# Performance work log

Hardware: AMD Instinct MI355X
Metric: run time of the kernel (lower is better)

The kernel has to match this reference:

```python
import jax, jax.numpy as jnp
import numpy as np

H = 2048        # hidden_size
NH = 16         # query heads
NKV = 4         # kv heads (= NH//4, from k_proj shape H x H//4)
HD = H // NH    # head_dim = 128
B, S = 2, 2048
SCALE = 1.0 / (HD ** 0.5)


def _rope(x, cos, sin):
    # x: [B, h, S, d]; cos/sin: [S, d//2]; rotate complex pairs (even, odd)
    xr = x[..., 0::2]
    xi = x[..., 1::2]
    c = cos[None, None, :x.shape[2], :]
    s = sin[None, None, :x.shape[2], :]
    out_r = xr * c - xi * s
    out_i = xr * s + xi * c
    return jnp.stack([out_r, out_i], axis=-1).reshape(x.shape)


def setup_inputs() -> dict:
    key = jax.random.key(0)
    ks = jax.random.split(key, 6)
    hidden_states = jax.random.normal(ks[0], (B, S, H), dtype=jnp.float32)
    # RoPE table (theta = 10000), head_dim//2 frequencies
    inv_freq = 1.0 / (10000.0 ** (np.arange(0, HD, 2, dtype=np.float32) / HD))
    angles = np.arange(S, dtype=np.float32)[:, None] * inv_freq[None, :]
    freqs_cos = jnp.asarray(np.cos(angles), dtype=jnp.float32)
    freqs_sin = jnp.asarray(np.sin(angles), dtype=jnp.float32)
    w = 0.02  # keep activations in a sane range
    Wq = jax.random.normal(ks[1], (H, H), dtype=jnp.float32) * w
    Wk = jax.random.normal(ks[2], (H // 4, H), dtype=jnp.float32) * w
    Wv = jax.random.normal(ks[3], (H // 4, H), dtype=jnp.float32) * w
    Wo = jax.random.normal(ks[4], (H, H), dtype=jnp.float32) * w
    return {"hidden_states": hidden_states, "freqs_cos": freqs_cos,
            "freqs_sin": freqs_sin, "Wq": Wq, "Wk": Wk, "Wv": Wv, "Wo": Wo}


def reference(hidden_states, freqs_cos, freqs_sin, Wq, Wk, Wv, Wo):
    b, s, _ = hidden_states.shape
    q = hidden_states @ Wq.T                      # [B,S,H]
    k = hidden_states @ Wk.T                      # [B,S,H/4]
    v = hidden_states @ Wv.T                      # [B,S,H/4]
    q = q.reshape(b, s, NH, HD).transpose(0, 2, 1, 3)    # [B,NH,S,HD]
    k = k.reshape(b, s, NKV, HD).transpose(0, 2, 1, 3)   # [B,NKV,S,HD]
    v = v.reshape(b, s, NKV, HD).transpose(0, 2, 1, 3)
    q = _rope(q, freqs_cos, freqs_sin)
    k = _rope(k, freqs_cos, freqs_sin)
    # GQA: each kv head serves NH//NKV query heads
    k_rep = jnp.repeat(k, NH // NKV, axis=1)      # [B,NH,S,HD]
    v_rep = jnp.repeat(v, NH // NKV, axis=1)
    scores = jnp.einsum('bhqd,bhkd->bhqk', q, k_rep) * SCALE  # [B,NH,S,S]
    probs = jax.nn.softmax(scores, axis=-1)
    out = jnp.einsum('bhqk,bhkd->bhqd', probs, v_rep)         # [B,NH,S,HD]
    out = out.transpose(0, 2, 1, 3).reshape(b, s, H)
    return out @ Wo.T
```

## Files before the change

kernel.cpp:

```cpp
#include <hip/hip_runtime.h>

typedef __bf16 bf16_t;
typedef bf16_t bf16x8 __attribute__((ext_vector_type(8)));
typedef bf16_t bf16x2 __attribute__((ext_vector_type(2)));
typedef float f32x4 __attribute__((ext_vector_type(4)));
typedef unsigned int u32x4 __attribute__((ext_vector_type(4)));

typedef const __attribute__((address_space(1))) void* as1_cvp;
typedef __attribute__((address_space(3))) void* as3_vp;

__device__ __forceinline__ void gload16(const void* g, void* l) {
  __builtin_amdgcn_global_load_lds((as1_cvp)g, (as3_vp)l, 16, 0, 0);
}

__global__ __launch_bounds__(256) void cvt_kernel(const float* __restrict__ src,
                                                  bf16_t* __restrict__ dst, int n8) {
  int i = blockIdx.x * 256 + threadIdx.x;
  if (i >= n8) return;
  int idx = i * 8;
  float4 a = *(const float4*)(src + idx);
  float4 b = *(const float4*)(src + idx + 4);
  bf16x8 o;
  o[0] = (bf16_t)a.x; o[1] = (bf16_t)a.y; o[2] = (bf16_t)a.z; o[3] = (bf16_t)a.w;
  o[4] = (bf16_t)b.x; o[5] = (bf16_t)b.y; o[6] = (bf16_t)b.z; o[7] = (bf16_t)b.w;
  *(bf16x8*)(dst + idx) = o;
}

#define BM 128
#define BN 128
#define BK 64
__global__ __launch_bounds__(256, 2) void gemm_bt(const bf16_t* __restrict__ A,
                                                  const bf16_t* __restrict__ B,
                                                  float* __restrict__ C,
                                                  int M, int N, int K) {
  __shared__ alignas(16) bf16_t As[BM * BK];
  __shared__ alignas(16) bf16_t Bs[BN * BK];
  const int t = threadIdx.x;
  const int lane = t & 63, w = t >> 6;
  const int wm = w >> 1, wn = w & 1;
  const int lr = lane & 15, lg = lane >> 4;
  const int m0 = blockIdx.y * BM, n0 = blockIdx.x * BN;
  const int srow = t >> 3, scol = (t & 7) * 8;

  f32x4 acc[4][4] = {};

  for (int kb = 0; kb < K; kb += BK) {
    __syncthreads();
#pragma unroll
    for (int i = 0; i < 4; ++i) {
      gload16(A + (size_t)(m0 + srow + 32 * i) * K + kb + scol, As + i * 2048 + t * 8);
      gload16(B + (size_t)(n0 + srow + 32 * i) * K + kb + scol, Bs + i * 2048 + t * 8);
    }
    __syncthreads();
#pragma unroll
    for (int kk = 0; kk < 2; ++kk) {
      const int ko = kk * 32 + lg * 8;
      bf16x8 af[4], bfr[4];
#pragma unroll
      for (int r = 0; r < 4; ++r)
        af[r] = *(const bf16x8*)(As + (wm * 64 + r * 16 + lr) * BK + ko);
#pragma unroll
      for (int c = 0; c < 4; ++c)
        bfr[c] = *(const bf16x8*)(Bs + (wn * 64 + c * 16 + lr) * BK + ko);
#pragma unroll
      for (int r = 0; r < 4; ++r)
#pragma unroll
        for (int c = 0; c < 4; ++c)
          acc[r][c] = __builtin_amdgcn_mfma_f32_16x16x32_bf16(af[r], bfr[c], acc[r][c], 0, 0, 0);
    }
  }
#pragma unroll
  for (int r = 0; r < 4; ++r)
#pragma unroll
    for (int c = 0; c < 4; ++c)
#pragma unroll
      for (int b = 0; b < 4; ++b)
        C[(size_t)(m0 + wm * 64 + r * 16 + lg * 4 + b) * N + n0 + wn * 64 + c * 16 + lr] =
            acc[r][c][b];
}

__global__ __launch_bounds__(256) void rope_kernel(const float* __restrict__ qkv,
                                                   const float* __restrict__ cs,
                                                   const float* __restrict__ sn,
                                                   bf16_t* __restrict__ dst,
                                                   int nh, int lognh, int col_off) {
  int idx = blockIdx.x * 256 + threadIdx.x;
  int chunk = idx & 15;
  int s = (idx >> 4) & 2047;
  int hh = (idx >> 15) & (nh - 1);
  int bb = idx >> (15 + lognh);
  const float* src = qkv + (size_t)(bb * 2048 + s) * 3072 + col_off + hh * 128 + chunk * 8;
  float4 x0 = *(const float4*)src;
  float4 x1 = *(const float4*)(src + 4);
  float4 c4 = *(const float4*)(cs + s * 64 + chunk * 4);
  float4 s4 = *(const float4*)(sn + s * 64 + chunk * 4);
  bf16x8 o;
  o[0] = (bf16_t)(x0.x * c4.x - x0.y * s4.x);
  o[1] = (bf16_t)(x0.x * s4.x + x0.y * c4.x);
  o[2] = (bf16_t)(x0.z * c4.y - x0.w * s4.y);
  o[3] = (bf16_t)(x0.z * s4.y + x0.w * c4.y);
  o[4] = (bf16_t)(x1.x * c4.z - x1.y * s4.z);
  o[5] = (bf16_t)(x1.x * s4.z + x1.y * c4.z);
  o[6] = (bf16_t)(x1.z * c4.w - x1.w * s4.w);
  o[7] = (bf16_t)(x1.z * s4.w + x1.w * c4.w);
  *(bf16x8*)(dst + ((size_t)(bb * nh + hh) * 2048 + s) * 128 + chunk * 8) = o;
}

__global__ __launch_bounds__(256) void vt_kernel(const float* __restrict__ qkv,
                                                 bf16_t* __restrict__ vt) {
  __shared__ bf16_t tile[64][128];
  int t = threadIdx.x;
  int bid = blockIdx.x;
  int st = bid & 31;
  int kh = (bid >> 5) & 3;
  int bb = bid >> 7;
  const float* src = qkv + (size_t)(bb * 2048 + st * 64) * 3072 + 2560 + kh * 128;
#pragma unroll
  for (int j = 0; j < 8; ++j) {
    int id = t + 256 * j;
    int sr = id >> 5, dv = id & 31;
    float4 x = *(const float4*)(src + (size_t)sr * 3072 + dv * 4);
    tile[sr][dv * 4 + 0] = (bf16_t)x.x;
    tile[sr][dv * 4 + 1] = (bf16_t)x.y;
    tile[sr][dv * 4 + 2] = (bf16_t)x.z;
    tile[sr][dv * 4 + 3] = (bf16_t)x.w;
  }
  __syncthreads();
  bf16_t* dst = vt + (size_t)(bb * 4 + kh) * 128 * 2048 + st * 64;
#pragma unroll
  for (int j = 0; j < 4; ++j) {
    int id = t + 256 * j;
    int d = id >> 3, sc8 = id & 7;
    bf16x8 v;
#pragma unroll
    for (int e = 0; e < 8; ++e) v[e] = tile[sc8 * 8 + e][d];
    *(bf16x8*)(dst + (size_t)d * 2048 + sc8 * 8) = v;
  }
}

#define KVB 64
__global__ __launch_bounds__(256, 3) void attn_kernel(const bf16_t* __restrict__ Q,
                                                      const bf16_t* __restrict__ Kg,
                                                      const bf16_t* __restrict__ Vg,
                                                      bf16_t* __restrict__ O) {
  __shared__ alignas(16) bf16_t Ks[2][KVB * 128];
  __shared__ alignas(16) bf16_t Vs[128 * KVB];
  const int t = threadIdx.x;
  const int lane = t & 63, w = t >> 6;
  const int lr = lane & 15, lg = lane >> 4;
  const int swz = (lr & 7) * 8;
  const int bid = blockIdx.x;
  const int qt = bid & 31;
  const int h = (bid >> 5) & 15;
  const int bb = bid >> 9;
  const int kvh = h >> 2;

  const bf16_t* Qh = Q + (((size_t)bb * 16 + h) * 2048 + qt * 64 + w * 16) * 128;
  const bf16_t* Kh = Kg + ((size_t)bb * 4 + kvh) * 2048 * 128;
  const bf16_t* Vh = Vg + ((size_t)bb * 4 + kvh) * 128 * 2048;

  const int krow = t >> 4;
  const int kcs = ((t & 15) ^ (krow & 7)) * 8;
  const int vrow = t >> 3;
  const int vcs = ((t & 7) ^ (vrow & 7)) * 8;

  bf16x8 qf[4];
#pragma unroll
  for (int kc = 0; kc < 4; ++kc)
    qf[kc] = *(const bf16x8*)(Qh + lr * 128 + kc * 32 + lg * 8);

  f32x4 o[8] = {};
  float m2 = -1e30f;
  float ls = 0.f;
  const float sm = 0.08838834764831845f * 1.44269504088896f;

#define STAGE_K(buf, kb)                                                                  \
  _Pragma("unroll") for (int i = 0; i < 4; ++i) {                                         \
    gload16(Kh + (size_t)((kb) + i * 16 + krow) * 128 + kcs, &Ks[buf][i * 2048 + t * 8]); \
  }
#define STAGE_V(kb)                                                                       \
  _Pragma("unroll") for (int i = 0; i < 4; ++i) {                                         \
    gload16(Vh + (size_t)(i * 32 + vrow) * 2048 + (kb) + vcs, &Vs[i * 2048 + t * 8]);     \
  }

  STAGE_K(0, 0);
  __syncthreads();

  for (int tt = 0; tt < 32; ++tt) {
    const int cur = tt & 1;
    const int kb = tt * KVB;
    STAGE_V(kb);
    if (tt < 31) { STAGE_K(cur ^ 1, kb + KVB); }
    const bf16_t* Kc = Ks[cur];

    f32x4 sc[4];
    __builtin_amdgcn_s_setprio(1);
#pragma unroll
    for (int cg = 0; cg < 4; ++cg) {
      f32x4 a = {};
#pragma unroll
      for (int kc = 0; kc < 4; ++kc) {
        bf16x8 kf = *(const bf16x8*)(Kc + (cg * 16 + lr) * 128 + ((kc * 32 + lg * 8) ^ swz));
        a = __builtin_amdgcn_mfma_f32_16x16x32_bf16(kf, qf[kc], a, 0, 0, 0);
      }
      sc[cg] = a * sm;
    }
    __builtin_amdgcn_s_setprio(0);

    float mx = fmaxf(fmaxf(fmaxf(sc[0][0], sc[0][1]), fmaxf(sc[0][2], sc[0][3])),
                     fmaxf(fmaxf(sc[1][0], sc[1][1]), fmaxf(sc[1][2], sc[1][3])));
    mx = fmaxf(mx, fmaxf(fmaxf(fmaxf(sc[2][0], sc[2][1]), fmaxf(sc[2][2], sc[2][3])),
                         fmaxf(fmaxf(sc[3][0], sc[3][1]), fmaxf(sc[3][2], sc[3][3]))));
    mx = fmaxf(mx, __shfl_xor(mx, 16));
    mx = fmaxf(mx, __shfl_xor(mx, 32));

    if (__any(mx > m2 + 8.0f)) {
      float mn = fmaxf(m2, mx);
      float resc = exp2f(m2 - mn);
      m2 = mn;
      ls *= resc;
      float rb[4];
#pragma unroll
      for (int b = 0; b < 4; ++b) rb[b] = __shfl(resc, lg * 4 + b);
#pragma unroll
      for (int d = 0; d < 8; ++d)
#pragma unroll
        for (int b = 0; b < 4; ++b) o[d][b] *= rb[b];
    }
#pragma unroll
    for (int cg = 0; cg < 4; ++cg)
#pragma unroll
      for (int b = 0; b < 4; ++b) {
        float p = exp2f(sc[cg][b] - m2);
        sc[cg][b] = p;
        ls += p;
      }

    unsigned W[8];
#pragma unroll
    for (int cg = 0; cg < 4; ++cg)
#pragma unroll
      for (int hh2 = 0; hh2 < 2; ++hh2) {
        bf16x2 pr = {(bf16_t)sc[cg][2 * hh2], (bf16_t)sc[cg][2 * hh2 + 1]};
        W[cg * 2 + hh2] = __builtin_bit_cast(unsigned, pr);
      }
    u32x4 pw[2];
#pragma unroll
    for (int kk = 0; kk < 2; ++kk)
#pragma unroll
      for (int m = 0; m < 4; ++m) {
        int srcl = lr + 16 * (2 * (lg & 1) + (m >> 1));
        int t0 = __shfl((int)W[(2 * kk) * 2 + (m & 1)], srcl);
        int t1 = __shfl((int)W[(2 * kk + 1) * 2 + (m & 1)], srcl);
        pw[kk][m] = (unsigned)((lg & 2) ? t1 : t0);
      }
    bf16x8 pf0 = __builtin_bit_cast(bf16x8, pw[0]);
    bf16x8 pf1 = __builtin_bit_cast(bf16x8, pw[1]);

    __syncthreads();

    __builtin_amdgcn_s_setprio(1);
#pragma unroll
    for (int d = 0; d < 8; ++d) {
      bf16x8 vf0 = *(const bf16x8*)(Vs + (d * 16 + lr) * KVB + ((0 * 32 + lg * 8) ^ swz));
      o[d] = __builtin_amdgcn_mfma_f32_16x16x32_bf16(pf0, vf0, o[d], 0, 0, 0);
      bf16x8 vf1 = *(const bf16x8*)(Vs + (d * 16 + lr) * KVB + ((1 * 32 + lg * 8) ^ swz));
      o[d] = __builtin_amdgcn_mfma_f32_16x16x32_bf16(pf1, vf1, o[d], 0, 0, 0);
    }
    __builtin_amdgcn_s_setprio(0);
    __syncthreads();
  }

  float lt = ls;
  lt += __shfl_xor(lt, 16);
  lt += __shfl_xor(lt, 32);
  float rinv[4];
#pragma unroll
  for (int b = 0; b < 4; ++b) rinv[b] = 1.0f / __shfl(lt, lg * 4 + b);
  const size_t q0 = (size_t)bb * 2048 + qt * 64 + w * 16;
#pragma unroll
  for (int d = 0; d < 8; ++d)
#pragma unroll
    for (int b = 0; b < 4; ++b) {
      float val = o[d][b] * rinv[b];
      O[(q0 + lg * 4 + b) * 2048 + h * 128 + d * 16 + lr] = (bf16_t)val;
    }
}

extern "C" void kernel_launch(void* const* d_in, const int* in_sizes, int n_in,
                              void* d_out, int out_size, void* d_ws, size_t ws_size,
                              hipStream_t stream) {
  const float* hs = (const float*)d_in[0];
  const float* fc = (const float*)d_in[1];
  const float* fs = (const float*)d_in[2];
  const float* Wq = (const float*)d_in[3];
  const float* Wk = (const float*)d_in[4];
  const float* Wv = (const float*)d_in[5];
  const float* Wo = (const float*)d_in[6];
  float* out = (float*)d_out;

  char* ws = (char*)d_ws;
  bf16_t* hs_b = (bf16_t*)ws;
  bf16_t* wcat = (bf16_t*)(ws + 16777216);
  bf16_t* wo_b = (bf16_t*)(ws + 29360128);
  float* qkv = (float*)(ws + 37748736);
  bf16_t* qr = (bf16_t*)(ws + 88080384);
  bf16_t* kr = (bf16_t*)(ws + 104857600);
  bf16_t* vt = (bf16_t*)(ws + 109051904);
  bf16_t* ao = (bf16_t*)(ws + 113246208);

  cvt_kernel<<<8388608 / 8 / 256, 256, 0, stream>>>(hs, hs_b, 8388608 / 8);
  cvt_kernel<<<4194304 / 8 / 256, 256, 0, stream>>>(Wq, wcat, 4194304 / 8);
  cvt_kernel<<<1048576 / 8 / 256, 256, 0, stream>>>(Wk, wcat + 4194304, 1048576 / 8);
  cvt_kernel<<<1048576 / 8 / 256, 256, 0, stream>>>(Wv, wcat + 5242880, 1048576 / 8);
  cvt_kernel<<<4194304 / 8 / 256, 256, 0, stream>>>(Wo, wo_b, 4194304 / 8);

  dim3 g1(3072 / BN, 4096 / BM);
  gemm_bt<<<g1, 256, 0, stream>>>(hs_b, wcat, qkv, 4096, 3072, 2048);

  rope_kernel<<<4096, 256, 0, stream>>>(qkv, fc, fs, qr, 16, 4, 0);
  rope_kernel<<<1024, 256, 0, stream>>>(qkv, fc, fs, kr, 4, 2, 2048);
  vt_kernel<<<256, 256, 0, stream>>>(qkv, vt);

  attn_kernel<<<1024, 256, 0, stream>>>(qr, kr, vt, ao);

  dim3 g2(2048 / BN, 4096 / BM);
  gemm_bt<<<g2, 256, 0, stream>>>(ao, wo_b, out, 4096, 2048, 2048);
}
```

Baseline: 299.5 us.

## Fuse RoPE and V transpose into QKV GEMM epilogue; restage attention K loads

The QKV projection GEMM now applies RoPE to the Q/K columns and writes bf16 straight into the head-major Q/K buffers. For the V columns it writes transposed bf16. This removes the fp32 qkv intermediate and three follow-up kernels. The attention kernel also drops the double-buffered K tile in LDS and prefetches K through registers into a single buffer, which allows higher occupancy (launch bounds 4). It also remaps block indices so that neighbouring blocks share KV heads. The epilogue's scattered 2-element and 4-element stores, plus the per-element cos/sin loads, may be less efficient than the separate kernels were.

```diff
diff --git a/kernel.cpp b/kernel.cpp
--- a/kernel.cpp
+++ b/kernel.cpp
@@ -2,6 +2,7 @@
 
 typedef __bf16 bf16_t;
 typedef bf16_t bf16x8 __attribute__((ext_vector_type(8)));
+typedef bf16_t bf16x4 __attribute__((ext_vector_type(4)));
 typedef bf16_t bf16x2 __attribute__((ext_vector_type(2)));
 typedef float f32x4 __attribute__((ext_vector_type(4)));
 typedef unsigned int u32x4 __attribute__((ext_vector_type(4)));
@@ -29,6 +30,7 @@
 #define BM 128
 #define BN 128
 #define BK 64
+
 __global__ __launch_bounds__(256, 2) void gemm_bt(const bf16_t* __restrict__ A,
                                                   const bf16_t* __restrict__ B,
                                                   float* __restrict__ C,
@@ -79,77 +81,107 @@
             acc[r][c][b];
 }
 
-__global__ __launch_bounds__(256) void rope_kernel(const float* __restrict__ qkv,
+__global__ __launch_bounds__(256, 2) void gemm_qkv(const bf16_t* __restrict__ A,
+                                                   const bf16_t* __restrict__ B,
                                                    const float* __restrict__ cs,
                                                    const float* __restrict__ sn,
-                                                   bf16_t* __restrict__ dst,
-                                                   int nh, int lognh, int col_off) {
-  int idx = blockIdx.x * 256 + threadIdx.x;
-  int chunk = idx & 15;
-  int s = (idx >> 4) & 2047;
-  int hh = (idx >> 15) & (nh - 1);
-  int bb = idx >> (15 + lognh);
-  const float* src = qkv + (size_t)(bb * 2048 + s) * 3072 + col_off + hh * 128 + chunk * 8;
-  float4 x0 = *(const float4*)src;
-  float4 x1 = *(const float4*)(src + 4);
-  float4 c4 = *(const float4*)(cs + s * 64 + chunk * 4);
-  float4 s4 = *(const float4*)(sn + s * 64 + chunk * 4);
-  bf16x8 o;
-  o[0] = (bf16_t)(x0.x * c4.x - x0.y * s4.x);
-  o[1] = (bf16_t)(x0.x * s4.x + x0.y * c4.x);
-  o[2] = (bf16_t)(x0.z * c4.y - x0.w * s4.y);
-  o[3] = (bf16_t)(x0.z * s4.y + x0.w * c4.y);
-  o[4] = (bf16_t)(x1.x * c4.z - x1.y * s4.z);
-  o[5] = (bf16_t)(x1.x * s4.z + x1.y * c4.z);
-  o[6] = (bf16_t)(x1.z * c4.w - x1.w * s4.w);
-  o[7] = (bf16_t)(x1.z * s4.w + x1.w * c4.w);
-  *(bf16x8*)(dst + ((size_t)(bb * nh + hh) * 2048 + s) * 128 + chunk * 8) = o;
-}
-
-__global__ __launch_bounds__(256) void vt_kernel(const float* __restrict__ qkv,
-                                                 bf16_t* __restrict__ vt) {
-  __shared__ bf16_t tile[64][128];
-  int t = threadIdx.x;
-  int bid = blockIdx.x;
-  int st = bid & 31;
-  int kh = (bid >> 5) & 3;
-  int bb = bid >> 7;
-  const float* src = qkv + (size_t)(bb * 2048 + st * 64) * 3072 + 2560 + kh * 128;
-#pragma unroll
-  for (int j = 0; j < 8; ++j) {
-    int id = t + 256 * j;
-    int sr = id >> 5, dv = id & 31;
-    float4 x = *(const float4*)(src + (size_t)sr * 3072 + dv * 4);
-    tile[sr][dv * 4 + 0] = (bf16_t)x.x;
-    tile[sr][dv * 4 + 1] = (bf16_t)x.y;
-    tile[sr][dv * 4 + 2] = (bf16_t)x.z;
-    tile[sr][dv * 4 + 3] = (bf16_t)x.w;
+                                                   bf16_t* __restrict__ qr,
+                                                   bf16_t* __restrict__ kr,
+                                                   bf16_t* __restrict__ vt) {
+  __shared__ alignas(16) bf16_t As[BM * BK];
+  __shared__ alignas(16) bf16_t Bs[BN * BK];
+  const int K = 2048;
+  const int t = threadIdx.x;
+  const int lane = t & 63, w = t >> 6;
+  const int wm = w >> 1, wn = w & 1;
+  const int lr = lane & 15, lg = lane >> 4;
+  const int m0 = blockIdx.y * BM, n0 = blockIdx.x * BN;
+  const int srow = t >> 3, scol = (t & 7) * 8;
+
+  f32x4 acc[4][4] = {};
+
+  for (int kb = 0; kb < K; kb += BK) {
+    __syncthreads();
+#pragma unroll
+    for (int i = 0; i < 4; ++i) {
+      gload16(A + (size_t)(m0 + srow + 32 * i) * K + kb + scol, As + i * 2048 + t * 8);
+      gload16(B + (size_t)(n0 + srow + 32 * i) * K + kb + scol, Bs + i * 2048 + t * 8);
+    }
+    __syncthreads();
+#pragma unroll
+    for (int kk = 0; kk < 2; ++kk) {
+      const int ko = kk * 32 + lg * 8;
+      bf16x8 af[4], bfr[4];
+#pragma unroll
+      for (int r = 0; r < 4; ++r)
+        af[r] = *(const bf16x8*)(As + (wm * 64 + r * 16 + lr) * BK + ko);
+#pragma unroll
+      for (int c = 0; c < 4; ++c)
+        bfr[c] = *(const bf16x8*)(Bs + (wn * 64 + c * 16 + lr) * BK + ko);
+#pragma unroll
+      for (int r = 0; r < 4; ++r)
+#pragma unroll
+        for (int c = 0; c < 4; ++c)
+          acc[r][c] = __builtin_amdgcn_mfma_f32_16x16x32_bf16(af[r], bfr[c], acc[r][c], 0, 0, 0);
+    }
   }
-  __syncthreads();
-  bf16_t* dst = vt + (size_t)(bb * 4 + kh) * 128 * 2048 + st * 64;
-#pragma unroll
-  for (int j = 0; j < 4; ++j) {
-    int id = t + 256 * j;
-    int d = id >> 3, sc8 = id & 7;
-    bf16x8 v;
-#pragma unroll
-    for (int e = 0; e < 8; ++e) v[e] = tile[sc8 * 8 + e][d];
-    *(bf16x8*)(dst + (size_t)d * 2048 + sc8 * 8) = v;
+
+  const int head = n0 >> 7;
+  const int bb2 = m0 >> 11;
+  const int sbase = (m0 & 2047) + wm * 64 + lg * 4;
+  if (head < 20) {
+    bf16_t* dst = (head < 16) ? qr + (size_t)(bb2 * 16 + head) * 2048 * 128
+                              : kr + (size_t)(bb2 * 4 + (head - 16)) * 2048 * 128;
+    const bool evn = (lr & 1) == 0;
+#pragma unroll
+    for (int r = 0; r < 4; ++r)
+#pragma unroll
+      for (int c = 0; c < 4; ++c) {
+        const int cw = wn * 64 + c * 16 + lr;
+        const int dix = cw >> 1;
+#pragma unroll
+        for (int b = 0; b < 4; ++b) {
+          const int s = sbase + r * 16 + b;
+          float own = acc[r][c][b];
+          float prt = __shfl_xor(own, 1);
+          if (evn) {
+            float cc = cs[s * 64 + dix];
+            float ssn = sn[s * 64 + dix];
+            bf16x2 pr;
+            pr[0] = (bf16_t)(own * cc - prt * ssn);
+            pr[1] = (bf16_t)(own * ssn + prt * cc);
+            *(bf16x2*)(dst + (size_t)s * 128 + cw) = pr;
+          }
+        }
+      }
+  } else {
+    bf16_t* dst = vt + (size_t)(bb2 * 4 + (head - 20)) * 128 * 2048;
+#pragma unroll
+    for (int r = 0; r < 4; ++r)
+#pragma unroll
+      for (int c = 0; c < 4; ++c) {
+        const int cw = wn * 64 + c * 16 + lr;
+        const int s = sbase + r * 16;
+        bf16x4 v4;
+#pragma unroll
+        for (int b = 0; b < 4; ++b) v4[b] = (bf16_t)acc[r][c][b];
+        *(bf16x4*)(dst + (size_t)cw * 2048 + s) = v4;
+      }
   }
 }
 
 #define KVB 64
-__global__ __launch_bounds__(256, 3) void attn_kernel(const bf16_t* __restrict__ Q,
+__global__ __launch_bounds__(256, 4) void attn_kernel(const bf16_t* __restrict__ Q,
                                                       const bf16_t* __restrict__ Kg,
                                                       const bf16_t* __restrict__ Vg,
                                                       bf16_t* __restrict__ O) {
-  __shared__ alignas(16) bf16_t Ks[2][KVB * 128];
+  __shared__ alignas(16) bf16_t Ks[KVB * 128];
   __shared__ alignas(16) bf16_t Vs[128 * KVB];
   const int t = threadIdx.x;
   const int lane = t & 63, w = t >> 6;
   const int lr = lane & 15, lg = lane >> 4;
   const int swz = (lr & 7) * 8;
-  const int bid = blockIdx.x;
+  const int bid = ((blockIdx.x & 7) << 7) | (blockIdx.x >> 3);
   const int qt = bid & 31;
   const int h = (bid >> 5) & 15;
   const int bb = bid >> 9;
@@ -174,25 +206,25 @@
   float ls = 0.f;
   const float sm = 0.08838834764831845f * 1.44269504088896f;
 
-#define STAGE_K(buf, kb)                                                                  \
-  _Pragma("unroll") for (int i = 0; i < 4; ++i) {                                         \
-    gload16(Kh + (size_t)((kb) + i * 16 + krow) * 128 + kcs, &Ks[buf][i * 2048 + t * 8]); \
-  }
-#define STAGE_V(kb)                                                                       \
-  _Pragma("unroll") for (int i = 0; i < 4; ++i) {                                         \
-    gload16(Vh + (size_t)(i * 32 + vrow) * 2048 + (kb) + vcs, &Vs[i * 2048 + t * 8]);     \
-  }
-
-  STAGE_K(0, 0);
+  bf16x8 kreg[4];
+
+#define KREG_LOAD(kb)                                                                   \
+  _Pragma("unroll") for (int i = 0; i < 4; ++i)                                         \
+    kreg[i] = *(const bf16x8*)(Kh + (size_t)((kb) + i * 16 + krow) * 128 + kcs);
+#define KDS_WRITE()                                                                     \
+  _Pragma("unroll") for (int i = 0; i < 4; ++i)                                         \
+    *(bf16x8*)(Ks + i * 2048 + t * 8) = kreg[i];
+#define STAGE_V(kb)                                                                     \
+  _Pragma("unroll") for (int i = 0; i < 4; ++i)                                         \
+    gload16(Vh + (size_t)(i * 32 + vrow) * 2048 + (kb) + vcs, Vs + i * 2048 + t * 8);
+
+  STAGE_V(0);
+  KREG_LOAD(0);
+  KDS_WRITE();
+  KREG_LOAD(KVB);
   __syncthreads();
 
   for (int tt = 0; tt < 32; ++tt) {
-    const int cur = tt & 1;
-    const int kb = tt * KVB;
-    STAGE_V(kb);
-    if (tt < 31) { STAGE_K(cur ^ 1, kb + KVB); }
-    const bf16_t* Kc = Ks[cur];
-
     f32x4 sc[4];
     __builtin_amdgcn_s_setprio(1);
 #pragma unroll
@@ -200,7 +232,7 @@
       f32x4 a = {};
 #pragma unroll
       for (int kc = 0; kc < 4; ++kc) {
-        bf16x8 kf = *(const bf16x8*)(Kc + (cg * 16 + lr) * 128 + ((kc * 32 + lg * 8) ^ swz));
+        bf16x8 kf = *(const bf16x8*)(Ks + (cg * 16 + lr) * 128 + ((kc * 32 + lg * 8) ^ swz));
         a = __builtin_amdgcn_mfma_f32_16x16x32_bf16(kf, qf[kc], a, 0, 0, 0);
       }
       sc[cg] = a * sm;
@@ -259,16 +291,21 @@
 
     __syncthreads();
 
+    if (tt < 31) { KDS_WRITE(); }
+
     __builtin_amdgcn_s_setprio(1);
 #pragma unroll
     for (int d = 0; d < 8; ++d) {
-      bf16x8 vf0 = *(const bf16x8*)(Vs + (d * 16 + lr) * KVB + ((0 * 32 + lg * 8) ^ swz));
+      bf16x8 vf0 = *(const bf16x8*)(Vs + (d * 16 + lr) * KVB + ((lg * 8) ^ swz));
       o[d] = __builtin_amdgcn_mfma_f32_16x16x32_bf16(pf0, vf0, o[d], 0, 0, 0);
-      bf16x8 vf1 = *(const bf16x8*)(Vs + (d * 16 + lr) * KVB + ((1 * 32 + lg * 8) ^ swz));
+      bf16x8 vf1 = *(const bf16x8*)(Vs + (d * 16 + lr) * KVB + ((32 + lg * 8) ^ swz));
       o[d] = __builtin_amdgcn_mfma_f32_16x16x32_bf16(pf1, vf1, o[d], 0, 0, 0);
     }
     __builtin_amdgcn_s_setprio(0);
     __syncthreads();
+
+    if (tt < 31) { STAGE_V((tt + 1) * KVB); }
+    if (tt < 30) { KREG_LOAD((tt + 2) * KVB); }
   }
 
   float lt = ls;
@@ -303,11 +340,10 @@
   bf16_t* hs_b = (bf16_t*)ws;
   bf16_t* wcat = (bf16_t*)(ws + 16777216);
   bf16_t* wo_b = (bf16_t*)(ws + 29360128);
-  float* qkv = (float*)(ws + 37748736);
-  bf16_t* qr = (bf16_t*)(ws + 88080384);
-  bf16_t* kr = (bf16_t*)(ws + 104857600);
-  bf16_t* vt = (bf16_t*)(ws + 109051904);
-  bf16_t* ao = (bf16_t*)(ws + 113246208);
+  bf16_t* qr = (bf16_t*)(ws + 37748736);
+  bf16_t* kr = (bf16_t*)(ws + 54525952);
+  bf16_t* vt = (bf16_t*)(ws + 58720256);
+  bf16_t* ao = (bf16_t*)(ws + 62914560);
 
   cvt_kernel<<<8388608 / 8 / 256, 256, 0, stream>>>(hs, hs_b, 8388608 / 8);
   cvt_kernel<<<4194304 / 8 / 256, 256, 0, stream>>>(Wq, wcat, 4194304 / 8);
@@ -316,11 +352,7 @@
   cvt_kernel<<<4194304 / 8 / 256, 256, 0, stream>>>(Wo, wo_b, 4194304 / 8);
 
   dim3 g1(3072 / BN, 4096 / BM);
-  gemm_bt<<<g1, 256, 0, stream>>>(hs_b, wcat, qkv, 4096, 3072, 2048);
-
-  rope_kernel<<<4096, 256, 0, stream>>>(qkv, fc, fs, qr, 16, 4, 0);
-  rope_kernel<<<1024, 256, 0, stream>>>(qkv, fc, fs, kr, 4, 2, 2048);
-  vt_kernel<<<256, 256, 0, stream>>>(qkv, vt);
+  gemm_qkv<<<g1, 256, 0, stream>>>(hs_b, wcat, fc, fs, qr, kr, vt);
 
   attn_kernel<<<1024, 256, 0, stream>>>(qr, kr, vt, ao);
 
```

Result: faster. 261.2 us (-12.8%).
